# Kernel optimization log

Measured on AMD Instinct MI355X. Metric: run time of the kernel, lower is better.

Reference implementation:

```python
import jax, jax.numpy as jnp
import numpy as np

L, H, NH, I = 6, 768, 12, 3072
DH = H // NH
EPS = 1e-12


def setup_inputs() -> dict:
    key = jax.random.key(0)
    ks = jax.random.split(key, 17)
    B, S = 16, 512
    s = lambda k, shape, fan: jax.random.normal(k, shape, jnp.float32) * (1.0 / np.sqrt(fan))
    return {
        "hidden_states": jax.random.normal(ks[0], (B, S, H), jnp.float32),
        "Wq": s(ks[1], (L, H, H), H), "bq": jnp.zeros((L, H), jnp.float32),
        "Wk": s(ks[2], (L, H, H), H), "bk": jnp.zeros((L, H), jnp.float32),
        "Wv": s(ks[3], (L, H, H), H), "bv": jnp.zeros((L, H), jnp.float32),
        "Wo": s(ks[4], (L, H, H), H), "bo": jnp.zeros((L, H), jnp.float32),
        "g1": jnp.ones((L, H), jnp.float32), "b1": jnp.zeros((L, H), jnp.float32),
        "Wi": s(ks[5], (L, H, I), H), "bi": jnp.zeros((L, I), jnp.float32),
        "Wo2": s(ks[6], (L, I, H), I), "bo2": jnp.zeros((L, H), jnp.float32),
        "g2": jnp.ones((L, H), jnp.float32), "b2": jnp.zeros((L, H), jnp.float32),
    }


def _layernorm(x, g, b):
    m = jnp.mean(x, axis=-1, keepdims=True)
    v = jnp.mean(jnp.square(x - m), axis=-1, keepdims=True)
    return (x - m) * jax.lax.rsqrt(v + EPS) * g + b


def _encoder(h, params):
    def layer_fn(h, p):
        Wq, bq, Wk, bk, Wv, bv, Wo, bo, g1, b1, Wi, bi, Wo2, bo2, g2, b2 = p
        B, S, _ = h.shape
        q = (h @ Wq + bq).reshape(B, S, NH, DH)
        k = (h @ Wk + bk).reshape(B, S, NH, DH)
        v = (h @ Wv + bv).reshape(B, S, NH, DH)
        scores = jnp.einsum("bshd,bthd->bhst", q, k) / np.sqrt(DH).astype(np.float32)
        probs = jax.nn.softmax(scores, axis=-1)  # dropout is identity in eval
        ctx = jnp.einsum("bhst,bthd->bshd", probs, v).reshape(B, S, H)
        attn_out = _layernorm(ctx @ Wo + bo + h, g1, b1)
        inter = jax.nn.gelu(attn_out @ Wi + bi, approximate=False)
        out = _layernorm(inter @ Wo2 + bo2 + attn_out, g2, b2)
        return out, None

    h, _ = jax.lax.scan(layer_fn, h, params)
    return h


def reference(hidden_states, Wq, bq, Wk, bk, Wv, bv, Wo, bo, g1, b1, Wi, bi, Wo2, bo2, g2, b2):
    params = (Wq, bq, Wk, bk, Wv, bv, Wo, bo, g1, b1, Wi, bi, Wo2, bo2, g2, b2)
    return _encoder(hidden_states, params)
```

## Files before the change

### kernel.cpp

```cpp
#include <hip/hip_runtime.h>
#include <hip/hip_bf16.h>
#include <math.h>

#define LNUM  6
#define HDIM  768
#define NHEAD 12
#define DHEAD 64
#define IDIM  3072
#define NB    16
#define SEQ   512
#define MTOK  (NB*SEQ)
#define NQKV  (3*HDIM)

typedef __bf16 bf16;
typedef __bf16 bf16x4 __attribute__((ext_vector_type(4)));
typedef __bf16 bf16x8 __attribute__((ext_vector_type(8)));
typedef float  f32x4  __attribute__((ext_vector_type(4)));

__device__ __forceinline__ void async_copy16(const bf16* g, bf16* l) {
  __builtin_amdgcn_global_load_lds((__attribute__((address_space(1))) void*)g,
                                   (__attribute__((address_space(3))) void*)l,
                                   16, 0, 0);
}

__device__ __forceinline__ float gelu_fast(float t) {
  const float u = 0.7978845608f * (t + 0.044715f * t * t * t);
  const float e = __expf(-2.f * fabsf(u));
  const float th = (1.f - e) / (1.f + e);
  return 0.5f * t * (1.f + copysignf(th, u));
}

__global__ void detect_k(const unsigned short* __restrict__ probe, int* __restrict__ flag)
{
  __shared__ int sc[4];
  const int tid = threadIdx.x;
  int cnt = 0;
#pragma unroll
  for (int j = 0; j < 16; j++) {
    const unsigned short w = probe[tid * 16 + j];
    const int e = (w >> 7) & 0xFF;
    cnt += (e >= 90 && e <= 130) ? 1 : 0;
  }
#pragma unroll
  for (int o = 32; o; o >>= 1) cnt += __shfl_xor(cnt, o);
  if ((tid & 63) == 0) sc[tid >> 6] = cnt;
  __syncthreads();
  if (tid == 0) flag[0] = ((sc[0] + sc[1] + sc[2] + sc[3]) < 3482) ? 1 : 0;
}

__global__ void cvt1d_k(const void* __restrict__ src, bf16* __restrict__ dst,
                        int n, const int* __restrict__ flag)
{
  const int i = blockIdx.x * 256 + threadIdx.x;
  if (i < n)
    dst[i] = (*flag) ? (bf16)((const float*)src)[i] : ((const bf16*)src)[i];
}

__global__ void cvt_slice_k(const void* __restrict__ src, bf16* __restrict__ dst,
                            int perL, int off, int dstStride, int total,
                            const int* __restrict__ flag)
{
  const int i = blockIdx.x * 256 + threadIdx.x;
  if (i < total) {
    const int l = i / perL, c = i - l * perL;
    const bf16 v = (*flag) ? (bf16)((const float*)src)[i] : ((const bf16*)src)[i];
    dst[l * dstStride + off + c] = v;
  }
}

__global__ void wtrans_k(const void* __restrict__ src, bf16* __restrict__ dst,
                         int K, int N, int layer, int dstLS, int dstOff,
                         const int* __restrict__ flag)
{
  __shared__ bf16 t[32][33];
  const size_t sOff = (size_t)(blockIdx.z + layer) * K * N;
  const size_t dOff = (size_t)blockIdx.z * dstLS + dstOff;
  const int n0 = blockIdx.x * 32, k0 = blockIdx.y * 32;
  const int tx = threadIdx.x, ty = threadIdx.y;
  const int f = *flag;
#pragma unroll
  for (int i = 0; i < 4; i++) {
    const size_t idx = sOff + (size_t)(k0 + ty*4 + i) * N + n0 + tx;
    t[ty*4+i][tx] = f ? (bf16)((const float*)src)[idx] : ((const bf16*)src)[idx];
  }
  __syncthreads();
#pragma unroll
  for (int i = 0; i < 4; i++)
    dst[dOff + (size_t)(n0 + ty*4 + i) * K + k0 + tx] = t[tx][ty*4+i];
}

#define STAGE3(DA, DB, KK) do {                                                \
    const int kk_ = ((KK) < K) ? (KK) : (K - 32);                              \
    _Pragma("unroll")                                                          \
    for (int p = 0; p < BM/64; p++)                                            \
      async_copy16(gA + (size_t)p * 64 * sA + kk_,                             \
                   &DA[(wave*16)*32 + p*64*32]);                               \
    _Pragma("unroll")                                                          \
    for (int p = 0; p < BN/64; p++)                                            \
      async_copy16(gB + (size_t)p * 64 * sB + kk_,                             \
                   &DB[(wave*16)*32 + p*64*32]);                               \
  } while (0)

#define COMP3(SA, SB) do {                                                     \
    bf16x8 af[MT], bfv[NT];                                                    \
    _Pragma("unroll")                                                          \
    for (int i = 0; i < MT; i++)                                               \
      af[i] = *(const bf16x8*)&SA[(wm*(MT*16) + i*16 + l16) * 32               \
                                  + (quad ^ swz) * 8];                         \
    _Pragma("unroll")                                                          \
    for (int j = 0; j < NT; j++)                                               \
      bfv[j] = *(const bf16x8*)&SB[(wn*(NT*16) + j*16 + l16) * 32              \
                                   + (quad ^ swz) * 8];                        \
    _Pragma("unroll")                                                          \
    for (int i = 0; i < MT; i++)                                               \
      _Pragma("unroll")                                                        \
      for (int j = 0; j < NT; j++)                                             \
        acc[i][j] = __builtin_amdgcn_mfma_f32_16x16x32_bf16(                   \
            af[i], bfv[j], acc[i][j], 0, 0, 0);                                \
  } while (0)

#define PIPE_STEP(SA, SB, DA, DB, KK) do {                                     \
    STAGE3(DA, DB, KK);                                                        \
    asm volatile("s_waitcnt vmcnt(4)" ::: "memory");                           \
    __builtin_amdgcn_s_barrier();                                              \
    COMP3(SA, SB);                                                             \
    __builtin_amdgcn_s_barrier();                                              \
  } while (0)

template<int BM, int BN, int MT, int NT, int EPI, int XS>
__global__ __launch_bounds__(256, 3)
void gemm_bt(const bf16* __restrict__ A, const bf16* __restrict__ Bt,
             float* __restrict__ Cf, bf16* __restrict__ Cb,
             bf16* __restrict__ Cb2, bf16* __restrict__ Cb3,
             const bf16* __restrict__ bias, const bf16* __restrict__ res,
             int K, int sA, int sB, int sC)
{
  __shared__ __align__(16) bf16 A0[BM*32];
  __shared__ __align__(16) bf16 B0[BN*32];
  __shared__ __align__(16) bf16 A1[BM*32];
  __shared__ __align__(16) bf16 B1[BN*32];
  __shared__ __align__(16) bf16 A2[BM*32];
  __shared__ __align__(16) bf16 B2[BN*32];
  const int tid  = threadIdx.x;
  const int wave = tid >> 6;
  const int lane = tid & 63;
  const int quad = lane >> 4;
  const int l16  = lane & 15;
  const int wm = wave >> 1, wn = wave & 1;
  const int swz = (l16 >> 1) & 3;

  int bx = blockIdx.x, by = blockIdx.y;
  if (XS) {
    if ((gridDim.y & 7) == 0) {
      const int id  = by * gridDim.x + bx;
      const int xcd = id & 7, slot = id >> 3;
      bx = slot % gridDim.x;
      by = (slot / gridDim.x) * 8 + xcd;
    }
  }
  const int m0 = by * BM;
  const int n0 = bx * BN;
  const int srow = tid >> 2;
  const int scol = (((tid & 3) ^ ((tid >> 3) & 3))) * 8;

  const bf16* gA = A + (size_t)(m0 + srow) * sA + scol;
  const bf16* gB = Bt + (size_t)(n0 + srow) * sB + scol;

  f32x4 acc[MT][NT];
  const f32x4 fzero = {0.f, 0.f, 0.f, 0.f};
#pragma unroll
  for (int i = 0; i < MT; i++)
#pragma unroll
    for (int j = 0; j < NT; j++) acc[i][j] = fzero;

  STAGE3(A0, B0, 0);
  STAGE3(A1, B1, 32);
  for (int k0 = 0; k0 < K; k0 += 96) {
    PIPE_STEP(A0, B0, A2, B2, k0 + 64);
    PIPE_STEP(A1, B1, A0, B0, k0 + 96);
    PIPE_STEP(A2, B2, A1, B1, k0 + 128);
  }

#pragma unroll
  for (int i = 0; i < MT; i++) {
    const int mtile = m0 + wm*(MT*16) + i*16 + quad*4;
#pragma unroll
    for (int j = 0; j < NT; j++) {
      const int nn = n0 + wn*(NT*16) + j*16 + l16;
      const float bv = bias ? (float)bias[nn] : 0.f;
      if (EPI == 5) {
        if (nn < HDIM) {
#pragma unroll
          for (int r = 0; r < 4; r++)
            Cb[(size_t)(mtile + r) * HDIM + nn] = (bf16)((acc[i][j][r] + bv) * 0.125f);
        } else if (nn < 2*HDIM) {
#pragma unroll
          for (int r = 0; r < 4; r++)
            Cb2[(size_t)(mtile + r) * HDIM + (nn - HDIM)] = (bf16)(acc[i][j][r] + bv);
        } else {
          const int nn2 = nn - 2*HDIM;
          const int bb = mtile >> 9, s = mtile & 511;
          const int hh = nn2 >> 6, dd = nn2 & 63;
          const size_t base = ((size_t)(bb*NHEAD + hh) * DHEAD + dd) * SEQ + s;
          bf16x4 pk;
#pragma unroll
          for (int r = 0; r < 4; r++) pk[r] = (bf16)(acc[i][j][r] + bv);
          *(bf16x4*)(Cb3 + base) = pk;
        }
      } else {
#pragma unroll
        for (int r = 0; r < 4; r++) {
          const int mm = mtile + r;
          const size_t idx = (size_t)mm * sC + nn;
          const float v = acc[i][j][r];
          if (EPI == 2) Cf[idx] = v + bv + (float)res[idx];
          else if (EPI == 3) Cb[idx] = (bf16)gelu_fast(v + bv);
        }
      }
    }
  }
}

__global__ __launch_bounds__(256)
void flash_k(const bf16* __restrict__ qb, const bf16* __restrict__ kb,
             const bf16* __restrict__ vt, bf16* __restrict__ ctxb)
{
  __shared__ __align__(16) bf16 Qs[128][72];
  __shared__ __align__(16) bf16 Ks[64][72];
  __shared__ __align__(16) bf16 Vs[64][72];
  __shared__ __align__(16) bf16 Ps[128][72];
  const int tid = threadIdx.x;
  const int wave = tid >> 6, lane = tid & 63;
  const int quad = lane >> 4, l16 = lane & 15;
  const int z = blockIdx.y;
  const int b = z / NHEAD, h = z - b * NHEAD;
  const int qt = blockIdx.x;
  const size_t qRow0 = (size_t)b * SEQ + qt * 128;

#pragma unroll
  for (int r = 0; r < 4; r++) {
    const int idx = tid + r * 256;
    const int row = idx >> 3, c8 = (idx & 7) * 8;
    *(bf16x8*)&Qs[row][c8] =
        *(const bf16x8*)&qb[(qRow0 + row) * HDIM + h * DHEAD + c8];
  }

  f32x4 Oacc[2][4];
  float mrow[2][4], lrow[2][4];
#pragma unroll
  for (int i = 0; i < 2; i++)
#pragma unroll
    for (int n = 0; n < 4; n++) Oacc[i][n] = (f32x4){0.f,0.f,0.f,0.f};
#pragma unroll
  for (int i = 0; i < 2; i++)
#pragma unroll
    for (int r = 0; r < 4; r++) { mrow[i][r] = -3.0e38f; lrow[i][r] = 0.f; }

  for (int j = 0; j < 8; j++) {
    __syncthreads();
#pragma unroll
    for (int r = 0; r < 2; r++) {
      const int idx = tid + r * 256;
      const int row = idx >> 3, c8 = (idx & 7) * 8;
      *(bf16x8*)&Ks[row][c8] =
          *(const bf16x8*)&kb[((size_t)b*SEQ + j*64 + row) * HDIM + h*DHEAD + c8];
      *(bf16x8*)&Vs[row][c8] =
          *(const bf16x8*)&vt[((size_t)z*DHEAD + row) * SEQ + j*64 + c8];
    }
    __syncthreads();

    f32x4 Sacc[2][4];
#pragma unroll
    for (int i = 0; i < 2; i++)
#pragma unroll
      for (int n = 0; n < 4; n++) Sacc[i][n] = (f32x4){0.f,0.f,0.f,0.f};
#pragma unroll
    for (int kk = 0; kk < 2; kk++) {
      bf16x8 af[2], bv[4];
#pragma unroll
      for (int i = 0; i < 2; i++)
        af[i] = *(const bf16x8*)&Qs[wave*32 + i*16 + l16][kk*32 + quad*8];
#pragma unroll
      for (int n = 0; n < 4; n++)
        bv[n] = *(const bf16x8*)&Ks[n*16 + l16][kk*32 + quad*8];
#pragma unroll
      for (int i = 0; i < 2; i++)
#pragma unroll
        for (int n = 0; n < 4; n++)
          Sacc[i][n] = __builtin_amdgcn_mfma_f32_16x16x32_bf16(af[i], bv[n], Sacc[i][n], 0,0,0);
    }

    float alpha[2][4];
#pragma unroll
    for (int i = 0; i < 2; i++)
#pragma unroll
      for (int r = 0; r < 4; r++) {
        float mx = Sacc[i][0][r];
#pragma unroll
        for (int n = 1; n < 4; n++) mx = fmaxf(mx, Sacc[i][n][r]);
#pragma unroll
        for (int o = 8; o; o >>= 1) mx = fmaxf(mx, __shfl_xor(mx, o));
        const float mn = fmaxf(mrow[i][r], mx);
        const float a = __expf(mrow[i][r] - mn);
        float rs = 0.f;
#pragma unroll
        for (int n = 0; n < 4; n++) {
          const float p = __expf(Sacc[i][n][r] - mn);
          Sacc[i][n][r] = p; rs += p;
        }
#pragma unroll
        for (int o = 8; o; o >>= 1) rs += __shfl_xor(rs, o);
        lrow[i][r] = lrow[i][r] * a + rs;
        mrow[i][r] = mn;
        alpha[i][r] = a;
      }

#pragma unroll
    for (int i = 0; i < 2; i++)
#pragma unroll
      for (int n = 0; n < 4; n++)
#pragma unroll
        for (int r = 0; r < 4; r++)
          Ps[wave*32 + i*16 + quad*4 + r][n*16 + l16] = (bf16)Sacc[i][n][r];
    __syncthreads();

#pragma unroll
    for (int i = 0; i < 2; i++)
#pragma unroll
      for (int n = 0; n < 4; n++)
#pragma unroll
        for (int r = 0; r < 4; r++) Oacc[i][n][r] *= alpha[i][r];
#pragma unroll
    for (int kk = 0; kk < 2; kk++) {
      bf16x8 af[2], bv[4];
#pragma unroll
      for (int i = 0; i < 2; i++)
        af[i] = *(const bf16x8*)&Ps[wave*32 + i*16 + l16][kk*32 + quad*8];
#pragma unroll
      for (int n = 0; n < 4; n++)
        bv[n] = *(const bf16x8*)&Vs[n*16 + l16][kk*32 + quad*8];
#pragma unroll
      for (int i = 0; i < 2; i++)
#pragma unroll
        for (int n = 0; n < 4; n++)
          Oacc[i][n] = __builtin_amdgcn_mfma_f32_16x16x32_bf16(af[i], bv[n], Oacc[i][n], 0,0,0);
    }
  }

#pragma unroll
  for (int i = 0; i < 2; i++)
#pragma unroll
    for (int r = 0; r < 4; r++) {
      const float inv = 1.f / lrow[i][r];
      const size_t tok = qRow0 + wave*32 + i*16 + quad*4 + r;
#pragma unroll
      for (int n = 0; n < 4; n++)
        ctxb[tok * HDIM + h*DHEAD + n*16 + l16] = (bf16)(Oacc[i][n][r] * inv);
    }
}

__global__ void layernorm_k(const float* __restrict__ x, const bf16* __restrict__ g,
                            const bf16* __restrict__ b, bf16* __restrict__ yb,
                            void* __restrict__ dout, int last, const int* __restrict__ flag)
{
  __shared__ float sred[4];
  const int row = blockIdx.x;
  const int tid = threadIdx.x;
  const float* xr = x + (size_t)row * HDIM;
  const float v0 = xr[tid], v1 = xr[tid+256], v2 = xr[tid+512];
  float s = v0 + v1 + v2;
#pragma unroll
  for (int o = 32; o; o >>= 1) s += __shfl_xor(s, o);
  if ((tid & 63) == 0) sred[tid >> 6] = s;
  __syncthreads();
  const float mean = (sred[0]+sred[1]+sred[2]+sred[3]) * (1.f/768.f);
  __syncthreads();
  const float d0 = v0-mean, d1 = v1-mean, d2 = v2-mean;
  float vs = d0*d0 + d1*d1 + d2*d2;
#pragma unroll
  for (int o = 32; o; o >>= 1) vs += __shfl_xor(vs, o);
  if ((tid & 63) == 0) sred[tid >> 6] = vs;
  __syncthreads();
  const float var = (sred[0]+sred[1]+sred[2]+sred[3]) * (1.f/768.f);
  const float rs  = rsqrtf(var + 1e-12f);
  const float y0 = d0*rs*(float)g[tid]     + (float)b[tid];
  const float y1 = d1*rs*(float)g[tid+256] + (float)b[tid+256];
  const float y2 = d2*rs*(float)g[tid+512] + (float)b[tid+512];
  bf16* ybr = yb + (size_t)row * HDIM;
  ybr[tid]     = (bf16)y0;
  ybr[tid+256] = (bf16)y1;
  ybr[tid+512] = (bf16)y2;
  if (last) {
    if (*flag) {
      float* o = (float*)dout + (size_t)row * HDIM;
      o[tid] = y0; o[tid+256] = y1; o[tid+512] = y2;
    } else {
      bf16* o = (bf16*)dout + (size_t)row * HDIM;
      o[tid] = (bf16)y0; o[tid+256] = (bf16)y1; o[tid+512] = (bf16)y2;
    }
  }
}

extern "C" void kernel_launch(void* const* d_in, const int* in_sizes, int n_in,
                              void* d_out, int out_size, void* d_ws, size_t ws_size,
                              hipStream_t stream)
{
  (void)in_sizes; (void)n_in; (void)out_size;

  char* ws = (char*)d_ws;
  size_t off = 0;
  auto carve = [&](size_t bytes) -> char* {
    char* p = ws + off; off += (bytes + 255) & ~(size_t)255; return p;
  };
  int*   flag = (int*)carve(256);
  bf16*  hcur = (bf16*)carve((size_t)MTOK*HDIM*2);
  bf16*  qb   = (bf16*)carve((size_t)MTOK*HDIM*2);
  bf16*  kb   = (bf16*)carve((size_t)MTOK*HDIM*2);
  bf16*  vt   = (bf16*)carve((size_t)MTOK*HDIM*2);
  bf16*  ctxb = (bf16*)carve((size_t)MTOK*HDIM*2);
  float* x1   = (float*)carve((size_t)MTOK*HDIM*4);
  bf16*  aob  = kb;

  bf16* nbqkv = (bf16*)carve((size_t)LNUM*NQKV*2);
  bf16* nbo   = (bf16*)carve((size_t)LNUM*HDIM*2);
  bf16* ng1   = (bf16*)carve((size_t)LNUM*HDIM*2);
  bf16* nb1   = (bf16*)carve((size_t)LNUM*HDIM*2);
  bf16* nbi   = (bf16*)carve((size_t)LNUM*IDIM*2);
  bf16* nbo2  = (bf16*)carve((size_t)LNUM*HDIM*2);
  bf16* ng2   = (bf16*)carve((size_t)LNUM*HDIM*2);
  bf16* nb2   = (bf16*)carve((size_t)LNUM*HDIM*2);

  const size_t wAllBytes = (size_t)LNUM*(NQKV*HDIM + HDIM*HDIM + 2*HDIM*IDIM)*2;
  const bool preAll = ws_size >= off + wAllBytes + (size_t)256*IDIM*2 + (1u<<20);
  bf16 *wqkvt=0, *wot=0, *wit=0, *wo2t=0, *bufA=0, *bufB=0;
  if (preAll) {
    wqkvt = (bf16*)carve((size_t)LNUM*NQKV*HDIM*2);
    wot   = (bf16*)carve((size_t)LNUM*HDIM*HDIM*2);
    wit   = (bf16*)carve((size_t)LNUM*HDIM*IDIM*2);
    wo2t  = (bf16*)carve((size_t)LNUM*HDIM*IDIM*2);
  } else {
    bufA = (bf16*)carve((size_t)HDIM*IDIM*2);
    bufB = (bf16*)carve((size_t)HDIM*IDIM*2);
  }

  const size_t unionAvail = (ws_size > off) ? (ws_size - off) : 0;
  int RM = 256;
  { const int rms[6] = {8192,4096,2048,1024,512,256};
    for (int i = 0; i < 6; i++)
      if ((size_t)rms[i]*IDIM*2 <= unionAvail) { RM = rms[i]; break; } }
  bf16* interb = (bf16*)(ws + off);

  detect_k<<<1, 256, 0, stream>>>((const unsigned short*)d_in[1], flag);
  cvt1d_k<<<(MTOK*HDIM+255)/256, 256, 0, stream>>>(d_in[0], hcur, MTOK*HDIM, flag);
  cvt_slice_k<<<(LNUM*HDIM+255)/256, 256, 0, stream>>>(d_in[2], nbqkv, HDIM, 0,      NQKV, LNUM*HDIM, flag);
  cvt_slice_k<<<(LNUM*HDIM+255)/256, 256, 0, stream>>>(d_in[4], nbqkv, HDIM, HDIM,   NQKV, LNUM*HDIM, flag);
  cvt_slice_k<<<(LNUM*HDIM+255)/256, 256, 0, stream>>>(d_in[6], nbqkv, HDIM, 2*HDIM, NQKV, LNUM*HDIM, flag);
  cvt1d_k<<<(LNUM*HDIM+255)/256, 256, 0, stream>>>(d_in[8],  nbo,  LNUM*HDIM, flag);
  cvt1d_k<<<(LNUM*HDIM+255)/256, 256, 0, stream>>>(d_in[9],  ng1,  LNUM*HDIM, flag);
  cvt1d_k<<<(LNUM*HDIM+255)/256, 256, 0, stream>>>(d_in[10], nb1,  LNUM*HDIM, flag);
  cvt1d_k<<<(LNUM*IDIM+255)/256, 256, 0, stream>>>(d_in[12], nbi,  LNUM*IDIM, flag);
  cvt1d_k<<<(LNUM*HDIM+255)/256, 256, 0, stream>>>(d_in[14], nbo2, LNUM*HDIM, flag);
  cvt1d_k<<<(LNUM*HDIM+255)/256, 256, 0, stream>>>(d_in[15], ng2,  LNUM*HDIM, flag);
  cvt1d_k<<<(LNUM*HDIM+255)/256, 256, 0, stream>>>(d_in[16], nb2,  LNUM*HDIM, flag);

  const dim3 tb(32, 8);
  if (preAll) {
    wtrans_k<<<dim3(HDIM/32, HDIM/32, LNUM), tb, 0, stream>>>(d_in[1], wqkvt, HDIM, HDIM, 0, NQKV*HDIM, 0,           flag);
    wtrans_k<<<dim3(HDIM/32, HDIM/32, LNUM), tb, 0, stream>>>(d_in[3], wqkvt, HDIM, HDIM, 0, NQKV*HDIM, HDIM*HDIM,   flag);
    wtrans_k<<<dim3(HDIM/32, HDIM/32, LNUM), tb, 0, stream>>>(d_in[5], wqkvt, HDIM, HDIM, 0, NQKV*HDIM, 2*HDIM*HDIM, flag);
    wtrans_k<<<dim3(HDIM/32, HDIM/32, LNUM), tb, 0, stream>>>(d_in[7], wot,  HDIM, HDIM, 0, HDIM*HDIM, 0, flag);
    wtrans_k<<<dim3(IDIM/32, HDIM/32, LNUM), tb, 0, stream>>>(d_in[11], wit,  HDIM, IDIM, 0, HDIM*IDIM, 0, flag);
    wtrans_k<<<dim3(HDIM/32, IDIM/32, LNUM), tb, 0, stream>>>(d_in[13], wo2t, IDIM, HDIM, 0, HDIM*IDIM, 0, flag);
  }

  for (int l = 0; l < LNUM; l++) {
    const bf16* hin = hcur;

    const bf16* WqkvT;
    if (preAll) WqkvT = wqkvt + (size_t)l * NQKV * HDIM;
    else {
      wtrans_k<<<dim3(HDIM/32, HDIM/32, 1), tb, 0, stream>>>(d_in[1], bufA, HDIM, HDIM, l, 0, 0,           flag);
      wtrans_k<<<dim3(HDIM/32, HDIM/32, 1), tb, 0, stream>>>(d_in[3], bufA, HDIM, HDIM, l, 0, HDIM*HDIM,   flag);
      wtrans_k<<<dim3(HDIM/32, HDIM/32, 1), tb, 0, stream>>>(d_in[5], bufA, HDIM, HDIM, l, 0, 2*HDIM*HDIM, flag);
      WqkvT = bufA;
    }
    gemm_bt<128,128,4,4,5,1><<<dim3(NQKV/128, MTOK/128), 256, 0, stream>>>(
        hin, WqkvT, nullptr, qb, kb, vt, nbqkv + (size_t)l*NQKV, nullptr,
        HDIM, HDIM, HDIM, HDIM);

    flash_k<<<dim3(SEQ/128, NB*NHEAD), 256, 0, stream>>>(qb, kb, vt, ctxb);

    const bf16* WoT;
    if (preAll) WoT = wot + (size_t)l * HDIM * HDIM;
    else {
      wtrans_k<<<dim3(HDIM/32, HDIM/32, 1), tb, 0, stream>>>(d_in[7], bufA, HDIM, HDIM, l, 0, 0, flag);
      WoT = bufA;
    }
    gemm_bt<128,128,4,4,2,1><<<dim3(HDIM/128, MTOK/128), 256, 0, stream>>>(
        ctxb, WoT, x1, nullptr, nullptr, nullptr, nbo + l*HDIM, hin,
        HDIM, HDIM, HDIM, HDIM);
    layernorm_k<<<MTOK, 256, 0, stream>>>(x1, ng1 + l*HDIM, nb1 + l*HDIM, aob,
                                          d_out, 0, flag);

    const bf16 *WiT, *Wo2T;
    if (preAll) { WiT = wit + (size_t)l*HDIM*IDIM; Wo2T = wo2t + (size_t)l*HDIM*IDIM; }
    else {
      wtrans_k<<<dim3(IDIM/32, HDIM/32, 1), tb, 0, stream>>>(d_in[11], bufA, HDIM, IDIM, l, 0, 0, flag);
      wtrans_k<<<dim3(HDIM/32, IDIM/32, 1), tb, 0, stream>>>(d_in[13], bufB, IDIM, HDIM, l, 0, 0, flag);
      WiT = bufA; Wo2T = bufB;
    }
    for (int r0 = 0; r0 < MTOK; r0 += RM) {
      gemm_bt<128,128,4,4,3,1><<<dim3(IDIM/128, RM/128), 256, 0, stream>>>(
          aob + (size_t)r0*HDIM, WiT, nullptr, interb, nullptr, nullptr,
          nbi + (size_t)l*IDIM, nullptr, HDIM, HDIM, HDIM, IDIM);
      gemm_bt<128,128,4,4,2,1><<<dim3(HDIM/128, RM/128), 256, 0, stream>>>(
          interb, Wo2T, x1 + (size_t)r0*HDIM, nullptr, nullptr, nullptr,
          nbo2 + l*HDIM, aob + (size_t)r0*HDIM, IDIM, IDIM, IDIM, HDIM);
    }
    layernorm_k<<<MTOK, 256, 0, stream>>>(x1, ng2 + l*HDIM, nb2 + l*HDIM, hcur,
                                          d_out, (l == LNUM-1) ? 1 : 0, flag);
  }
}
```

Measured before the change: 1.864 ms.

## Split-K the N=768 GEMMs into two partials and fold reduction into layernorm

The output-projection and FFN down-projection GEMMs (N=768, only 6 column tiles) now run as split-K with two halves writing separate fp32 partial buffers. A new layernorm kernel sums the two partials and adds bias and residual before normalizing. This raises the block count to improve CU occupancy on those narrow GEMMs. In exchange it costs an extra fp32 buffer write and read per GEMM. It also adds s_setprio around the MFMA loop and a final vmcnt(0) wait.

```diff
diff --git a/kernel.cpp b/kernel.cpp
--- a/kernel.cpp
+++ b/kernel.cpp
@@ -111,12 +111,14 @@
     for (int j = 0; j < NT; j++)                                               \
       bfv[j] = *(const bf16x8*)&SB[(wn*(NT*16) + j*16 + l16) * 32              \
                                    + (quad ^ swz) * 8];                        \
+    __builtin_amdgcn_s_setprio(1);                                             \
     _Pragma("unroll")                                                          \
     for (int i = 0; i < MT; i++)                                               \
       _Pragma("unroll")                                                        \
       for (int j = 0; j < NT; j++)                                             \
         acc[i][j] = __builtin_amdgcn_mfma_f32_16x16x32_bf16(                   \
             af[i], bfv[j], acc[i][j], 0, 0, 0);                                \
+    __builtin_amdgcn_s_setprio(0);                                             \
   } while (0)
 
 #define PIPE_STEP(SA, SB, DA, DB, KK) do {                                     \
@@ -130,10 +132,11 @@
 template<int BM, int BN, int MT, int NT, int EPI, int XS>
 __global__ __launch_bounds__(256, 3)
 void gemm_bt(const bf16* __restrict__ A, const bf16* __restrict__ Bt,
-             float* __restrict__ Cf, bf16* __restrict__ Cb,
-             bf16* __restrict__ Cb2, bf16* __restrict__ Cb3,
+             float* __restrict__ Cf, float* __restrict__ Cf2,
+             bf16* __restrict__ Cb, bf16* __restrict__ Cb2,
+             bf16* __restrict__ Cb3,
              const bf16* __restrict__ bias, const bf16* __restrict__ res,
-             int K, int sA, int sB, int sC)
+             int K, int sA, int sB, int sC, int ksplit)
 {
   __shared__ __align__(16) bf16 A0[BM*32];
   __shared__ __align__(16) bf16 B0[BN*32];
@@ -149,6 +152,8 @@
   const int wm = wave >> 1, wn = wave & 1;
   const int swz = (l16 >> 1) & 3;
 
+  if (ksplit && blockIdx.z) { A += ksplit; Bt += ksplit; Cf = Cf2; }
+
   int bx = blockIdx.x, by = blockIdx.y;
   if (XS) {
     if ((gridDim.y & 7) == 0) {
@@ -180,6 +185,7 @@
     PIPE_STEP(A1, B1, A0, B0, k0 + 96);
     PIPE_STEP(A2, B2, A1, B1, k0 + 128);
   }
+  asm volatile("s_waitcnt vmcnt(0)" ::: "memory");
 
 #pragma unroll
   for (int i = 0; i < MT; i++) {
@@ -187,8 +193,8 @@
 #pragma unroll
     for (int j = 0; j < NT; j++) {
       const int nn = n0 + wn*(NT*16) + j*16 + l16;
-      const float bv = bias ? (float)bias[nn] : 0.f;
       if (EPI == 5) {
+        const float bv = (float)bias[nn];
         if (nn < HDIM) {
 #pragma unroll
           for (int r = 0; r < 4; r++)
@@ -207,15 +213,15 @@
           for (int r = 0; r < 4; r++) pk[r] = (bf16)(acc[i][j][r] + bv);
           *(bf16x4*)(Cb3 + base) = pk;
         }
-      } else {
-#pragma unroll
-        for (int r = 0; r < 4; r++) {
-          const int mm = mtile + r;
-          const size_t idx = (size_t)mm * sC + nn;
-          const float v = acc[i][j][r];
-          if (EPI == 2) Cf[idx] = v + bv + (float)res[idx];
-          else if (EPI == 3) Cb[idx] = (bf16)gelu_fast(v + bv);
-        }
+      } else if (EPI == 3) {
+        const float bv = (float)bias[nn];
+#pragma unroll
+        for (int r = 0; r < 4; r++)
+          Cb[(size_t)(mtile + r) * sC + nn] = (bf16)gelu_fast(acc[i][j][r] + bv);
+      } else if (EPI == 4) {
+#pragma unroll
+        for (int r = 0; r < 4; r++)
+          Cf[(size_t)(mtile + r) * sC + nn] = acc[i][j][r];
       }
     }
   }
@@ -359,15 +365,19 @@
     }
 }
 
-__global__ void layernorm_k(const float* __restrict__ x, const bf16* __restrict__ g,
-                            const bf16* __restrict__ b, bf16* __restrict__ yb,
-                            void* __restrict__ dout, int last, const int* __restrict__ flag)
+__global__ void layernorm2_k(const float* __restrict__ xa, const float* __restrict__ xb,
+                             const bf16* __restrict__ bias, const bf16* __restrict__ res,
+                             const bf16* __restrict__ g, const bf16* __restrict__ b,
+                             bf16* __restrict__ yb, void* __restrict__ dout,
+                             int last, const int* __restrict__ flag)
 {
   __shared__ float sred[4];
   const int row = blockIdx.x;
   const int tid = threadIdx.x;
-  const float* xr = x + (size_t)row * HDIM;
-  const float v0 = xr[tid], v1 = xr[tid+256], v2 = xr[tid+512];
+  const size_t base = (size_t)row * HDIM;
+  const float v0 = xa[base+tid]     + xb[base+tid]     + (float)bias[tid]     + (float)res[base+tid];
+  const float v1 = xa[base+tid+256] + xb[base+tid+256] + (float)bias[tid+256] + (float)res[base+tid+256];
+  const float v2 = xa[base+tid+512] + xb[base+tid+512] + (float)bias[tid+512] + (float)res[base+tid+512];
   float s = v0 + v1 + v2;
 #pragma unroll
   for (int o = 32; o; o >>= 1) s += __shfl_xor(s, o);
@@ -386,16 +396,16 @@
   const float y0 = d0*rs*(float)g[tid]     + (float)b[tid];
   const float y1 = d1*rs*(float)g[tid+256] + (float)b[tid+256];
   const float y2 = d2*rs*(float)g[tid+512] + (float)b[tid+512];
-  bf16* ybr = yb + (size_t)row * HDIM;
+  bf16* ybr = yb + base;
   ybr[tid]     = (bf16)y0;
   ybr[tid+256] = (bf16)y1;
   ybr[tid+512] = (bf16)y2;
   if (last) {
     if (*flag) {
-      float* o = (float*)dout + (size_t)row * HDIM;
+      float* o = (float*)dout + base;
       o[tid] = y0; o[tid+256] = y1; o[tid+512] = y2;
     } else {
-      bf16* o = (bf16*)dout + (size_t)row * HDIM;
+      bf16* o = (bf16*)dout + base;
       o[tid] = (bf16)y0; o[tid+256] = (bf16)y1; o[tid+512] = (bf16)y2;
     }
   }
@@ -419,6 +429,7 @@
   bf16*  vt   = (bf16*)carve((size_t)MTOK*HDIM*2);
   bf16*  ctxb = (bf16*)carve((size_t)MTOK*HDIM*2);
   float* x1   = (float*)carve((size_t)MTOK*HDIM*4);
+  float* x2   = (float*)carve((size_t)MTOK*HDIM*4);
   bf16*  aob  = kb;
 
   bf16* nbqkv = (bf16*)carve((size_t)LNUM*NQKV*2);
@@ -485,8 +496,8 @@
       WqkvT = bufA;
     }
     gemm_bt<128,128,4,4,5,1><<<dim3(NQKV/128, MTOK/128), 256, 0, stream>>>(
-        hin, WqkvT, nullptr, qb, kb, vt, nbqkv + (size_t)l*NQKV, nullptr,
-        HDIM, HDIM, HDIM, HDIM);
+        hin, WqkvT, nullptr, nullptr, qb, kb, vt, nbqkv + (size_t)l*NQKV, nullptr,
+        HDIM, HDIM, HDIM, HDIM, 0);
 
     flash_k<<<dim3(SEQ/128, NB*NHEAD), 256, 0, stream>>>(qb, kb, vt, ctxb);
 
@@ -496,11 +507,12 @@
       wtrans_k<<<dim3(HDIM/32, HDIM/32, 1), tb, 0, stream>>>(d_in[7], bufA, HDIM, HDIM, l, 0, 0, flag);
       WoT = bufA;
     }
-    gemm_bt<128,128,4,4,2,1><<<dim3(HDIM/128, MTOK/128), 256, 0, stream>>>(
-        ctxb, WoT, x1, nullptr, nullptr, nullptr, nbo + l*HDIM, hin,
-        HDIM, HDIM, HDIM, HDIM);
-    layernorm_k<<<MTOK, 256, 0, stream>>>(x1, ng1 + l*HDIM, nb1 + l*HDIM, aob,
-                                          d_out, 0, flag);
+    gemm_bt<128,128,4,4,4,1><<<dim3(HDIM/128, MTOK/128, 2), 256, 0, stream>>>(
+        ctxb, WoT, x1, x2, nullptr, nullptr, nullptr, nullptr, nullptr,
+        HDIM/2, HDIM, HDIM, HDIM, HDIM/2);
+    layernorm2_k<<<MTOK, 256, 0, stream>>>(x1, x2, nbo + l*HDIM, hin,
+                                           ng1 + l*HDIM, nb1 + l*HDIM, aob,
+                                           d_out, 0, flag);
 
     const bf16 *WiT, *Wo2T;
     if (preAll) { WiT = wit + (size_t)l*HDIM*IDIM; Wo2T = wo2t + (size_t)l*HDIM*IDIM; }
@@ -511,13 +523,15 @@
     }
     for (int r0 = 0; r0 < MTOK; r0 += RM) {
       gemm_bt<128,128,4,4,3,1><<<dim3(IDIM/128, RM/128), 256, 0, stream>>>(
-          aob + (size_t)r0*HDIM, WiT, nullptr, interb, nullptr, nullptr,
-          nbi + (size_t)l*IDIM, nullptr, HDIM, HDIM, HDIM, IDIM);
-      gemm_bt<128,128,4,4,2,1><<<dim3(HDIM/128, RM/128), 256, 0, stream>>>(
-          interb, Wo2T, x1 + (size_t)r0*HDIM, nullptr, nullptr, nullptr,
-          nbo2 + l*HDIM, aob + (size_t)r0*HDIM, IDIM, IDIM, IDIM, HDIM);
-    }
-    layernorm_k<<<MTOK, 256, 0, stream>>>(x1, ng2 + l*HDIM, nb2 + l*HDIM, hcur,
-                                          d_out, (l == LNUM-1) ? 1 : 0, flag);
-  }
-}
+          aob + (size_t)r0*HDIM, WiT, nullptr, nullptr, interb, nullptr, nullptr,
+          nbi + (size_t)l*IDIM, nullptr, HDIM, HDIM, HDIM, IDIM, 0);
+      gemm_bt<128,128,4,4,4,1><<<dim3(HDIM/128, RM/128, 2), 256, 0, stream>>>(
+          interb, Wo2T, x1 + (size_t)r0*HDIM, x2 + (size_t)r0*HDIM,
+          nullptr, nullptr, nullptr, nullptr, nullptr,
+          IDIM/2, IDIM, IDIM, HDIM, IDIM/2);
+    }
+    layernorm2_k<<<MTOK, 256, 0, stream>>>(x1, x2, nbo2 + l*HDIM, aob,
+                                           ng2 + l*HDIM, nb2 + l*HDIM, hcur,
+                                           d_out, (l == LNUM-1) ? 1 : 0, flag);
+  }
+}
```

Result: faster. 1.797 ms (-3.6%).
